# Optimization experiments

Hardware: AMD Instinct MI355X
Metric: run time of the kernel (lower is better)

The kernel has to match this reference:

```python
import jax, jax.numpy as jnp
import numpy as np


def _gru(x_seq, W_ih, W_hh, b_ih, b_hh):
    """Batched torch-style GRU. x_seq: [B,T,H] -> outputs [B,T,H].
    Gate order (torch.nn.GRU): r, z, n. n = tanh(xn + r*(W_hn h + b_hn))."""
    B, T, H = x_seq.shape
    # precompute input projections for all timesteps: [B,T,3H]
    xp = jnp.einsum('bth,gh->btg', x_seq, W_ih) + b_ih

    def step(h, xt):  # h: [B,H], xt: [B,3H]
        hp = h @ W_hh.T + b_hh  # [B,3H]
        xr, xz, xn = jnp.split(xt, 3, axis=-1)
        hr, hz, hn = jnp.split(hp, 3, axis=-1)
        r = jax.nn.sigmoid(xr + hr)
        z = jax.nn.sigmoid(xz + hz)
        n = jnp.tanh(xn + r * hn)
        h_new = (1.0 - z) * n + z * h
        return h_new, h_new

    h0 = jnp.zeros((B, H), dtype=x_seq.dtype)
    _, hs = jax.lax.scan(step, h0, jnp.swapaxes(xp, 0, 1))  # [T,B,H]
    return jnp.swapaxes(hs, 0, 1)


def setup_inputs() -> dict:
    key = jax.random.key(0)
    B, T, C, H, D = 128, 64, 8000, 256, 16
    G = 3 * H
    ks = jax.random.split(key, 32)
    s = 0.05  # scale for stable params
    inp = {
        'x': (jax.random.uniform(ks[0], (B, T, C)) < 0.01).astype(jnp.float32),  # sparse multi-hot
        'demographic': jax.random.normal(ks[1], (B, D), jnp.float32),
        'embed_W': jax.random.normal(ks[2], (H, C), jnp.float32) * s,
        'embed_b': jax.random.normal(ks[3], (H,), jnp.float32) * s,
        'aW_ih': jax.random.normal(ks[4], (G, H), jnp.float32) * s,
        'aW_hh': jax.random.normal(ks[5], (G, H), jnp.float32) * s,
        'ab_ih': jax.random.normal(ks[6], (G,), jnp.float32) * s,
        'ab_hh': jax.random.normal(ks[7], (G,), jnp.float32) * s,
        'bW_ih': jax.random.normal(ks[8], (G, H), jnp.float32) * s,
        'bW_hh': jax.random.normal(ks[9], (G, H), jnp.float32) * s,
        'bb_ih': jax.random.normal(ks[10], (G,), jnp.float32) * s,
        'bb_hh': jax.random.normal(ks[11], (G,), jnp.float32) * s,
        'attnA_W': jax.random.normal(ks[12], (1, H), jnp.float32) * s,
        'attnA_b': jax.random.normal(ks[13], (1,), jnp.float32) * s,
        'attnB_W': jax.random.normal(ks[14], (H, H), jnp.float32) * s,
        'attnB_b': jax.random.normal(ks[15], (H,), jnp.float32) * s,
        'cls_W1': jax.random.normal(ks[16], (H, H + D), jnp.float32) * s,
        'cls_b1': jax.random.normal(ks[17], (H,), jnp.float32) * s,
        'cls_W2': jax.random.normal(ks[18], (C, H), jnp.float32) * s,
        'cls_b2': jax.random.normal(ks[19], (C,), jnp.float32) * s,
        'dl_W1': jax.random.normal(ks[20], (H, H + D), jnp.float32) * s,
        'dl_b1': jax.random.normal(ks[21], (H,), jnp.float32) * s,
        'dl_W2': jax.random.normal(ks[22], (1, H), jnp.float32) * s,
        'dl_b2': jax.random.normal(ks[23], (1,), jnp.float32) * s,
    }
    return inp


def reference(x, demographic, embed_W, embed_b,
              aW_ih, aW_hh, ab_ih, ab_hh,
              bW_ih, bW_hh, bb_ih, bb_hh,
              attnA_W, attnA_b, attnB_W, attnB_b,
              cls_W1, cls_b1, cls_W2, cls_b2,
              dl_W1, dl_b1, dl_W2, dl_b2):
    # code embedding: [B,T,C] @ [C,H] -> [B,T,H]
    embedded = jnp.einsum('btc,hc->bth', x, embed_W) + embed_b

    alpha_out = _gru(embedded, aW_ih, aW_hh, ab_ih, ab_hh)  # [B,T,H]
    beta_out = _gru(embedded, bW_ih, bW_hh, bb_ih, bb_hh)   # [B,T,H]

    e_alpha = jnp.einsum('bth,oh->bto', alpha_out, attnA_W)[..., 0] + attnA_b[0]  # [B,T]
    alpha = jax.nn.softmax(e_alpha, axis=1)                                       # [B,T]
    beta = jnp.tanh(jnp.einsum('bth,gh->btg', beta_out, attnB_W) + attnB_b)       # [B,T,H]

    context = jnp.einsum('bth,bt->bh', embedded * beta, alpha)  # [B,H]

    combined = jnp.concatenate([context, demographic], axis=1)  # [B,H+D]
    # classifier (dropout = identity, eval mode)
    h1 = jax.nn.relu(combined @ cls_W1.T + cls_b1)
    logits = h1 @ cls_W2.T + cls_b2                              # [B,C]
    # death/LOS head
    h2 = jax.nn.relu(combined @ dl_W1.T + dl_b1)
    dl_logit = h2 @ dl_W2.T + dl_b2                              # [B,1]

    return jnp.concatenate([logits, dl_logit], axis=1)          # [B,C+1]
```

## Files before the change

### kernel.cpp

```cpp
#include <hip/hip_runtime.h>


typedef __attribute__((ext_vector_type(4))) float f32x4;
typedef __attribute__((ext_vector_type(8))) short short8;

__device__ inline short f2bf(float f) {
  unsigned u = __float_as_uint(f);
  u += 0x7fffu + ((u >> 16) & 1u);
  return (short)(u >> 16);
}
__device__ inline float bf2f(short u) {
  return __uint_as_float(((unsigned)(unsigned short)u) << 16);
}
__device__ inline float sigf(float x) { return 1.f / (1.f + __expf(-x)); }
__device__ inline float tanh_fast(float x) {
  x = fminf(fmaxf(x, -15.f), 15.f);
  float e = __expf(2.f * x);
  return (e - 1.f) / (e + 1.f);
}

__global__ void transpose_w(const float* __restrict__ in, float* __restrict__ outT) {
  __shared__ float tile[32][33];
  const int tx = threadIdx.x, ty = threadIdx.y;
  const int c0 = blockIdx.x * 32, h0 = blockIdx.y * 32;
#pragma unroll
  for (int k = 0; k < 4; ++k)
    tile[ty * 4 + k][tx] = in[(long)(h0 + ty * 4 + k) * 8000 + c0 + tx];
  __syncthreads();
#pragma unroll
  for (int k = 0; k < 4; ++k)
    outT[(long)(c0 + ty * 4 + k) * 256 + h0 + tx] = tile[tx][ty * 4 + k];
}

__global__ __launch_bounds__(512) void pad_pack(const float* __restrict__ w1,
                                                const float* __restrict__ w1d,
                                                float* __restrict__ o1,
                                                float* __restrict__ o2,
                                                const float* __restrict__ aWhh,
                                                const float* __restrict__ bWhh,
                                                short* __restrict__ wbf) {
  const int bid = blockIdx.x;
  if (bid < 288) {
    int idx = bid * 512 + threadIdx.x;
    int half = idx / (256 * 288);
    int r = idx % (256 * 288);
    int n = r / 288, k = r % 288;
    float v = (k < 272) ? (half ? w1d[n * 272 + k] : w1[n * 272 + k]) : 0.f;
    if (half) o2[r] = v; else o1[r] = v;
  } else {
    const int F = (bid - 288) * 512 + threadIdx.x;
    int f = F;
    const int lane = f & 63; f >>= 6;
    const int w = f & 15; f >>= 4;
    const int e = f % 3; f /= 3;
    const int kt = f & 7; f >>= 3;
    const int gru = f;
    const float* W = gru ? bWhh : aWhh;
    const int g = e * 256 + w * 16 + (lane & 15);
    const int k = kt * 32 + (lane >> 4) * 8;
    const float* p = W + (long)g * 256 + k;
    short8 v;
#pragma unroll
    for (int j = 0; j < 8; ++j) v[j] = f2bf(p[j]);
    *(short8*)(wbf + (long)F * 8) = v;
  }
}

__global__ __launch_bounds__(256) void embed_sparse(const float* __restrict__ x,
                                                    const float* __restrict__ Wt,
                                                    const float* __restrict__ eb,
                                                    float* __restrict__ emb) {
  __shared__ int sidx[512];
  __shared__ float sval[512];
  __shared__ int scnt;
  const int bt = blockIdx.x;
  const int tid = threadIdx.x;
  if (tid == 0) scnt = 0;
  __syncthreads();
  const float* xr = x + (long)bt * 8000;
  for (int i = tid; i < 2000; i += 256) {
    float4 v = ((const float4*)xr)[i];
    if (v.x != 0.f) { int p = atomicAdd(&scnt, 1); if (p < 512) { sidx[p] = i * 4 + 0; sval[p] = v.x; } }
    if (v.y != 0.f) { int p = atomicAdd(&scnt, 1); if (p < 512) { sidx[p] = i * 4 + 1; sval[p] = v.y; } }
    if (v.z != 0.f) { int p = atomicAdd(&scnt, 1); if (p < 512) { sidx[p] = i * 4 + 2; sval[p] = v.z; } }
    if (v.w != 0.f) { int p = atomicAdd(&scnt, 1); if (p < 512) { sidx[p] = i * 4 + 3; sval[p] = v.w; } }
  }
  __syncthreads();
  const int n = min(scnt, 512);
  float acc = eb[tid];
  for (int i = 0; i < n; ++i) acc += sval[i] * Wt[(long)sidx[i] * 256 + tid];
  emb[(long)bt * 256 + tid] = acc;
}

__global__ __launch_bounds__(256) void gemm_bt(const float* __restrict__ A,
                                               const float* __restrict__ B,
                                               const float* __restrict__ bias,
                                               float* __restrict__ C,
                                               int M, int N, int K, int ldc, int act) {
  __shared__ short As[64][40];
  __shared__ short Bs[64][40];
  const int tid = threadIdx.x;
  const int lane = tid & 63, wave = tid >> 6;
  const int wm = wave >> 1, wn = wave & 1;
  const int l15 = lane & 15, lhi = lane >> 4;
  const int m0 = blockIdx.y * 64, n0 = blockIdx.x * 64;
  const int srow = tid >> 2, scol = (tid & 3) * 8;
  f32x4 acc[2][2];
#pragma unroll
  for (int i = 0; i < 2; ++i)
#pragma unroll
    for (int j = 0; j < 2; ++j) acc[i][j] = (f32x4){0.f, 0.f, 0.f, 0.f};

  for (int k0 = 0; k0 < K; k0 += 32) {
    __syncthreads();
    {
      const float* p = A + (long)(m0 + srow) * K + k0 + scol;
      float4 f0 = *(const float4*)p;
      float4 f1 = *(const float4*)(p + 4);
      short8 v;
      v[0] = f2bf(f0.x); v[1] = f2bf(f0.y); v[2] = f2bf(f0.z); v[3] = f2bf(f0.w);
      v[4] = f2bf(f1.x); v[5] = f2bf(f1.y); v[6] = f2bf(f1.z); v[7] = f2bf(f1.w);
      *(short8*)&As[srow][scol] = v;
      const float* q = B + (long)(n0 + srow) * K + k0 + scol;
      float4 g0 = *(const float4*)q;
      float4 g1 = *(const float4*)(q + 4);
      short8 u;
      u[0] = f2bf(g0.x); u[1] = f2bf(g0.y); u[2] = f2bf(g0.z); u[3] = f2bf(g0.w);
      u[4] = f2bf(g1.x); u[5] = f2bf(g1.y); u[6] = f2bf(g1.z); u[7] = f2bf(g1.w);
      *(short8*)&Bs[srow][scol] = u;
    }
    __syncthreads();
    short8 af0 = *(const short8*)&As[wm * 32 + l15][lhi * 8];
    short8 af1 = *(const short8*)&As[wm * 32 + 16 + l15][lhi * 8];
    short8 bf0 = *(const short8*)&Bs[wn * 32 + l15][lhi * 8];
    short8 bf1 = *(const short8*)&Bs[wn * 32 + 16 + l15][lhi * 8];
    acc[0][0] = __builtin_amdgcn_mfma_f32_16x16x32_bf16(af0, bf0, acc[0][0], 0, 0, 0);
    acc[0][1] = __builtin_amdgcn_mfma_f32_16x16x32_bf16(af0, bf1, acc[0][1], 0, 0, 0);
    acc[1][0] = __builtin_amdgcn_mfma_f32_16x16x32_bf16(af1, bf0, acc[1][0], 0, 0, 0);
    acc[1][1] = __builtin_amdgcn_mfma_f32_16x16x32_bf16(af1, bf1, acc[1][1], 0, 0, 0);
  }
#pragma unroll
  for (int j = 0; j < 2; ++j) {
    const int col = n0 + wn * 32 + j * 16 + l15;
    const float bv = bias[col];
#pragma unroll
    for (int i = 0; i < 2; ++i) {
#pragma unroll
      for (int r = 0; r < 4; ++r) {
        const int row = m0 + wm * 32 + i * 16 + lhi * 4 + r;
        float v = acc[i][j][r] + bv;
        if (act == 1) v = fmaxf(v, 0.f);
        else if (act == 2) v = tanh_fast(v);
        C[(long)row * ldc + col] = v;
      }
    }
  }
}

__global__ __launch_bounds__(256) void gemm_dual(const float* __restrict__ A,
                                                 const float* __restrict__ B1,
                                                 const float* __restrict__ B2,
                                                 const float* __restrict__ bias1,
                                                 const float* __restrict__ bias2,
                                                 short* __restrict__ C1,
                                                 short* __restrict__ C2,
                                                 int K) {
  __shared__ short As[64][40];
  __shared__ short Bs1[64][40];
  __shared__ short Bs2[64][40];
  const int tid = threadIdx.x;
  const int lane = tid & 63, wave = tid >> 6;
  const int wm = wave >> 1, wn = wave & 1;
  const int l15 = lane & 15, lhi = lane >> 4;
  const int m0 = blockIdx.y * 64, n0 = blockIdx.x * 64;
  const int srow = tid >> 2, scol = (tid & 3) * 8;
  f32x4 acc1[2][2], acc2[2][2];
#pragma unroll
  for (int i = 0; i < 2; ++i)
#pragma unroll
    for (int j = 0; j < 2; ++j) {
      acc1[i][j] = (f32x4){0.f, 0.f, 0.f, 0.f};
      acc2[i][j] = (f32x4){0.f, 0.f, 0.f, 0.f};
    }

  for (int k0 = 0; k0 < K; k0 += 32) {
    __syncthreads();
    {
      const float* p = A + (long)(m0 + srow) * K + k0 + scol;
      float4 f0 = *(const float4*)p;
      float4 f1 = *(const float4*)(p + 4);
      short8 v;
      v[0] = f2bf(f0.x); v[1] = f2bf(f0.y); v[2] = f2bf(f0.z); v[3] = f2bf(f0.w);
      v[4] = f2bf(f1.x); v[5] = f2bf(f1.y); v[6] = f2bf(f1.z); v[7] = f2bf(f1.w);
      *(short8*)&As[srow][scol] = v;
      const float* q1 = B1 + (long)(n0 + srow) * K + k0 + scol;
      float4 g0 = *(const float4*)q1;
      float4 g1 = *(const float4*)(q1 + 4);
      short8 u;
      u[0] = f2bf(g0.x); u[1] = f2bf(g0.y); u[2] = f2bf(g0.z); u[3] = f2bf(g0.w);
      u[4] = f2bf(g1.x); u[5] = f2bf(g1.y); u[6] = f2bf(g1.z); u[7] = f2bf(g1.w);
      *(short8*)&Bs1[srow][scol] = u;
      const float* q2 = B2 + (long)(n0 + srow) * K + k0 + scol;
      float4 h0 = *(const float4*)q2;
      float4 h1 = *(const float4*)(q2 + 4);
      short8 t;
      t[0] = f2bf(h0.x); t[1] = f2bf(h0.y); t[2] = f2bf(h0.z); t[3] = f2bf(h0.w);
      t[4] = f2bf(h1.x); t[5] = f2bf(h1.y); t[6] = f2bf(h1.z); t[7] = f2bf(h1.w);
      *(short8*)&Bs2[srow][scol] = t;
    }
    __syncthreads();
    short8 af0 = *(const short8*)&As[wm * 32 + l15][lhi * 8];
    short8 af1 = *(const short8*)&As[wm * 32 + 16 + l15][lhi * 8];
    short8 b10 = *(const short8*)&Bs1[wn * 32 + l15][lhi * 8];
    short8 b11 = *(const short8*)&Bs1[wn * 32 + 16 + l15][lhi * 8];
    short8 b20 = *(const short8*)&Bs2[wn * 32 + l15][lhi * 8];
    short8 b21 = *(const short8*)&Bs2[wn * 32 + 16 + l15][lhi * 8];
    acc1[0][0] = __builtin_amdgcn_mfma_f32_16x16x32_bf16(af0, b10, acc1[0][0], 0, 0, 0);
    acc1[0][1] = __builtin_amdgcn_mfma_f32_16x16x32_bf16(af0, b11, acc1[0][1], 0, 0, 0);
    acc1[1][0] = __builtin_amdgcn_mfma_f32_16x16x32_bf16(af1, b10, acc1[1][0], 0, 0, 0);
    acc1[1][1] = __builtin_amdgcn_mfma_f32_16x16x32_bf16(af1, b11, acc1[1][1], 0, 0, 0);
    acc2[0][0] = __builtin_amdgcn_mfma_f32_16x16x32_bf16(af0, b20, acc2[0][0], 0, 0, 0);
    acc2[0][1] = __builtin_amdgcn_mfma_f32_16x16x32_bf16(af0, b21, acc2[0][1], 0, 0, 0);
    acc2[1][0] = __builtin_amdgcn_mfma_f32_16x16x32_bf16(af1, b20, acc2[1][0], 0, 0, 0);
    acc2[1][1] = __builtin_amdgcn_mfma_f32_16x16x32_bf16(af1, b21, acc2[1][1], 0, 0, 0);
  }
#pragma unroll
  for (int j = 0; j < 2; ++j) {
    const int col = n0 + wn * 32 + j * 16 + l15;
    const float bv1 = bias1[col];
    const float bv2 = bias2[col];
#pragma unroll
    for (int i = 0; i < 2; ++i) {
#pragma unroll
      for (int r = 0; r < 4; ++r) {
        const int row = m0 + wm * 32 + i * 16 + lhi * 4 + r;
        C1[(long)row * 768 + col] = f2bf(acc1[i][j][r] + bv1);
        C2[(long)row * 768 + col] = f2bf(acc2[i][j][r] + bv2);
      }
    }
  }
}

__global__ __launch_bounds__(1024, 4)
void gru_scan(const short* __restrict__ xpa,
              const short* __restrict__ xpb,
              const short* __restrict__ wbf,
              const float* __restrict__ abhh,
              const float* __restrict__ bbhh,
              float* __restrict__ aout,
              float* __restrict__ bout) {
  const int tid = threadIdx.x;
  const int lane = tid & 63, w = tid >> 6;
  const int l15 = lane & 15, lhi = lane >> 4;
  const int gru = blockIdx.x >> 5, chunk = blockIdx.x & 31;
  const int b0 = chunk * 4;
  const short* xp  = gru ? xpb : xpa;
  const float* bhh = gru ? bbhh : abhh;
  float* outp = gru ? bout : aout;

  __shared__ short hl[2][16][264];
  __shared__ short xplb[2][4][768];
  __shared__ short wlds[16][3][64][8];

  auto FR = [&](int kt, int e) -> const short8* {
    return (const short8*)(wbf + ((((long)gru * 8 + kt) * 3 + e) * 16 + w) * 512 + (long)lane * 8);
  };

  short8 wf[3][5];
#pragma unroll
  for (int e = 0; e < 3; ++e)
#pragma unroll
    for (int kt = 0; kt < 5; ++kt) wf[e][kt] = *FR(kt, e);
#pragma unroll
  for (int e = 0; e < 3; ++e) *(short8*)&wlds[w][e][lane][0] = *FR(5, e);

  float bh[3];
#pragma unroll
  for (int e = 0; e < 3; ++e) bh[e] = bhh[e * 256 + w * 16 + l15];

  for (int i = tid; i < 2 * 16 * 264; i += 1024) (&hl[0][0][0])[i] = 0;

  auto STAGE = [&](int par, int tt) {
    if (w < 6) {
      const int c = w * 64 + lane;
      const int b = c / 96, off8 = (c % 96) * 8;
      const short* gp = xp + ((long)(b0 + b) * 64 + tt) * 768 + off8;
      __builtin_amdgcn_global_load_lds((const __attribute__((address_space(1))) unsigned int*)gp,
                                       (__attribute__((address_space(3))) unsigned int*)((short*)&xplb[par][0][0] + (long)w * 512),
                                       16, 0, 0);
    }
  };
  STAGE(0, 0);
  __syncthreads();

  float hreg = 0.f;
  const int col = w * 16 + l15;

  for (int t = 0; t < 64; ++t) {
    const int cur = t & 1;
    short8 s60 = *FR(6, 0), s61 = *FR(6, 1), s62 = *FR(6, 2);
    short8 s70 = *FR(7, 0), s71 = *FR(7, 1), s72 = *FR(7, 2);
    if (t + 1 < 64) STAGE(cur ^ 1, t + 1);

    f32x4 acc[3];
#pragma unroll
    for (int e = 0; e < 3; ++e) acc[e] = (f32x4){0.f, 0.f, 0.f, 0.f};
#pragma unroll
    for (int kt = 0; kt < 5; ++kt) {
      short8 a = *(const short8*)&hl[cur][l15][kt * 32 + lhi * 8];
      acc[0] = __builtin_amdgcn_mfma_f32_16x16x32_bf16(a, wf[0][kt], acc[0], 0, 0, 0);
      acc[1] = __builtin_amdgcn_mfma_f32_16x16x32_bf16(a, wf[1][kt], acc[1], 0, 0, 0);
      acc[2] = __builtin_amdgcn_mfma_f32_16x16x32_bf16(a, wf[2][kt], acc[2], 0, 0, 0);
    }
    {
      short8 a = *(const short8*)&hl[cur][l15][5 * 32 + lhi * 8];
#pragma unroll
      for (int e = 0; e < 3; ++e) {
        short8 wl = *(const short8*)&wlds[w][e][lane][0];
        acc[e] = __builtin_amdgcn_mfma_f32_16x16x32_bf16(a, wl, acc[e], 0, 0, 0);
      }
    }
    {
      short8 a = *(const short8*)&hl[cur][l15][6 * 32 + lhi * 8];
      acc[0] = __builtin_amdgcn_mfma_f32_16x16x32_bf16(a, s60, acc[0], 0, 0, 0);
      acc[1] = __builtin_amdgcn_mfma_f32_16x16x32_bf16(a, s61, acc[1], 0, 0, 0);
      acc[2] = __builtin_amdgcn_mfma_f32_16x16x32_bf16(a, s62, acc[2], 0, 0, 0);
    }
    {
      short8 a = *(const short8*)&hl[cur][l15][7 * 32 + lhi * 8];
      acc[0] = __builtin_amdgcn_mfma_f32_16x16x32_bf16(a, s70, acc[0], 0, 0, 0);
      acc[1] = __builtin_amdgcn_mfma_f32_16x16x32_bf16(a, s71, acc[1], 0, 0, 0);
      acc[2] = __builtin_amdgcn_mfma_f32_16x16x32_bf16(a, s72, acc[2], 0, 0, 0);
    }

    {
      const float xr = bf2f(xplb[cur][lhi][col]);
      const float xz = bf2f(xplb[cur][lhi][256 + col]);
      const float xn = bf2f(xplb[cur][lhi][512 + col]);
      const float r = sigf(xr + acc[0][0] + bh[0]);
      const float z = sigf(xz + acc[1][0] + bh[1]);
      const float n = tanh_fast(xn + r * (acc[2][0] + bh[2]));
      const float hn = (1.f - z) * n + z * hreg;
      hreg = hn;
      hl[cur ^ 1][lhi << 2][col] = f2bf(hn);
      outp[((long)(b0 + lhi) * 64 + t) * 256 + col] = hn;
    }
    __syncthreads();
  }
}

__global__ __launch_bounds__(256) void alpha_ctx(const float* __restrict__ aout,
                                                 const float* __restrict__ aW,
                                                 const float* __restrict__ ab,
                                                 const float* __restrict__ emb,
                                                 const float* __restrict__ beta,
                                                 const float* __restrict__ demo,
                                                 float* __restrict__ comb) {
  __shared__ float part[64][4];
  __shared__ float al[64];
  const int b = blockIdx.x, tid = threadIdx.x;
  const int t = tid >> 2, q = tid & 3;
  const float* p = aout + (long)(b * 64 + t) * 256 + q * 64;
  const float* wv = aW + q * 64;
  float s = 0.f;
  for (int i = 0; i < 64; ++i) s += p[i] * wv[i];
  part[t][q] = s;
  __syncthreads();
  if (tid < 64) {
    float e = part[tid][0] + part[tid][1] + part[tid][2] + part[tid][3] + ab[0];
    float m = e;
    for (int k = 32; k; k >>= 1) m = fmaxf(m, __shfl_xor(m, k));
    float ex = __expf(e - m);
    float sum = ex;
    for (int k = 32; k; k >>= 1) sum += __shfl_xor(sum, k);
    al[tid] = ex / sum;
  }
  __syncthreads();
  const int h = tid;
  float acc = 0.f;
  for (int t2 = 0; t2 < 64; ++t2) {
    const long ix = (long)(b * 64 + t2) * 256 + h;
    acc += al[t2] * emb[ix] * beta[ix];
  }
  comb[b * 288 + h] = acc;
  if (h < 16) comb[b * 288 + 256 + h] = demo[b * 16 + h];
  else if (h < 32) comb[b * 288 + 256 + h] = 0.f;
}

__global__ __launch_bounds__(64) void dl_head(const float* __restrict__ h2,
                                              const float* __restrict__ w,
                                              const float* __restrict__ bias,
                                              float* __restrict__ out) {
  const int b = blockIdx.x, lane = threadIdx.x;
  float s = 0.f;
#pragma unroll
  for (int i = 0; i < 4; ++i) s += h2[b * 256 + lane * 4 + i] * w[lane * 4 + i];
  for (int k = 32; k; k >>= 1) s += __shfl_xor(s, k);
  if (lane == 0) out[(long)b * 8001 + 8000] = s + bias[0];
}

extern "C" void kernel_launch(void* const* d_in, const int* in_sizes, int n_in,
                              void* d_out, int out_size, void* d_ws, size_t ws_size,
                              hipStream_t stream) {
  (void)in_sizes; (void)n_in; (void)out_size; (void)ws_size;
  const float* x      = (const float*)d_in[0];
  const float* demo   = (const float*)d_in[1];
  const float* embW   = (const float*)d_in[2];
  const float* embB   = (const float*)d_in[3];
  const float* aWih   = (const float*)d_in[4];
  const float* aWhh   = (const float*)d_in[5];
  const float* abih   = (const float*)d_in[6];
  const float* abhh   = (const float*)d_in[7];
  const float* bWih   = (const float*)d_in[8];
  const float* bWhh   = (const float*)d_in[9];
  const float* bbih   = (const float*)d_in[10];
  const float* bbhh   = (const float*)d_in[11];
  const float* attnAW = (const float*)d_in[12];
  const float* attnAb = (const float*)d_in[13];
  const float* attnBW = (const float*)d_in[14];
  const float* attnBb = (const float*)d_in[15];
  const float* clsW1  = (const float*)d_in[16];
  const float* clsb1  = (const float*)d_in[17];
  const float* clsW2  = (const float*)d_in[18];
  const float* clsb2  = (const float*)d_in[19];
  const float* dlW1   = (const float*)d_in[20];
  const float* dlb1   = (const float*)d_in[21];
  const float* dlW2   = (const float*)d_in[22];
  const float* dlb2   = (const float*)d_in[23];
  float* out = (float*)d_out;
  float* ws = (float*)d_ws;

  float* Wt    = ws;
  float* emb   = Wt + 2048000;
  short* xpa16 = (short*)(emb + 2097152);
  short* xpb16 = xpa16 + 6291456;
  float* aoutB = (float*)(xpb16 + 6291456);
  float* boutB = aoutB + 2097152;
  float* betaB = boutB + 2097152;
  float* comb  = betaB + 2097152;
  float* h1    = comb + 36864;
  float* h2    = h1 + 32768;
  float* W1p   = h2 + 32768;
  float* W1pd  = W1p + 73728;
  short* wbf   = (short*)(W1pd + 73728);

  transpose_w<<<dim3(250, 8), dim3(32, 8), 0, stream>>>(embW, Wt);
  pad_pack<<<dim3(384), dim3(512), 0, stream>>>(clsW1, dlW1, W1p, W1pd, aWhh, bWhh, wbf);
  embed_sparse<<<dim3(8192), dim3(256), 0, stream>>>(x, Wt, embB, emb);
  gemm_dual<<<dim3(12, 128), dim3(256), 0, stream>>>(emb, aWih, bWih, abih, bbih, xpa16, xpb16, 256);
  gru_scan<<<dim3(64), dim3(1024), 0, stream>>>(xpa16, xpb16, wbf, abhh, bbhh, aoutB, boutB);
  gemm_bt<<<dim3(4, 128), dim3(256), 0, stream>>>(boutB, attnBW, attnBb, betaB, 8192, 256, 256, 256, 2);
  alpha_ctx<<<dim3(128), dim3(256), 0, stream>>>(aoutB, attnAW, attnAb, emb, betaB, demo, comb);
  gemm_bt<<<dim3(4, 2), dim3(256), 0, stream>>>(comb, W1p, clsb1, h1, 128, 256, 288, 256, 1);
  gemm_bt<<<dim3(4, 2), dim3(256), 0, stream>>>(comb, W1pd, dlb1, h2, 128, 256, 288, 256, 1);
  gemm_bt<<<dim3(125, 2), dim3(256), 0, stream>>>(h1, clsW2, clsb2, out, 128, 8000, 256, 8001, 0);
  dl_head<<<dim3(128), dim3(64), 0, stream>>>(h2, dlW2, dlb2, out);
}
```

Before: 267.0 us.

## Store intermediates in bf16 and pre-convert GEMM weights once

Measured after the change: 255.4 us. -4.4%, faster.

```diff
diff --git a/kernel.cpp b/kernel.cpp
--- a/kernel.cpp
+++ b/kernel.cpp
@@ -38,7 +38,13 @@
                                                 float* __restrict__ o2,
                                                 const float* __restrict__ aWhh,
                                                 const float* __restrict__ bWhh,
-                                                short* __restrict__ wbf) {
+                                                short* __restrict__ wbf,
+                                                const float* __restrict__ aWih,
+                                                const float* __restrict__ bWih,
+                                                const float* __restrict__ attnBW,
+                                                short* __restrict__ wih16a,
+                                                short* __restrict__ wih16b,
+                                                short* __restrict__ attnBW16) {
   const int bid = blockIdx.x;
   if (bid < 288) {
     int idx = bid * 512 + threadIdx.x;
@@ -47,7 +53,7 @@
     int n = r / 288, k = r % 288;
     float v = (k < 272) ? (half ? w1d[n * 272 + k] : w1[n * 272 + k]) : 0.f;
     if (half) o2[r] = v; else o1[r] = v;
-  } else {
+  } else if (bid < 384) {
     const int F = (bid - 288) * 512 + threadIdx.x;
     int f = F;
     const int lane = f & 63; f >>= 6;
@@ -63,13 +69,18 @@
 #pragma unroll
     for (int j = 0; j < 8; ++j) v[j] = f2bf(p[j]);
     *(short8*)(wbf + (long)F * 8) = v;
+  } else {
+    const int i = (bid - 384) * 512 + threadIdx.x;
+    if (i < 196608) wih16a[i] = f2bf(aWih[i]);
+    else if (i < 393216) wih16b[i - 196608] = f2bf(bWih[i - 196608]);
+    else attnBW16[i - 393216] = f2bf(attnBW[i - 393216]);
   }
 }
 
 __global__ __launch_bounds__(256) void embed_sparse(const float* __restrict__ x,
                                                     const float* __restrict__ Wt,
                                                     const float* __restrict__ eb,
-                                                    float* __restrict__ emb) {
+                                                    short* __restrict__ emb16) {
   __shared__ int sidx[512];
   __shared__ float sval[512];
   __shared__ int scnt;
@@ -89,7 +100,7 @@
   const int n = min(scnt, 512);
   float acc = eb[tid];
   for (int i = 0; i < n; ++i) acc += sval[i] * Wt[(long)sidx[i] * 256 + tid];
-  emb[(long)bt * 256 + tid] = acc;
+  emb16[(long)bt * 256 + tid] = f2bf(acc);
 }
 
 __global__ __launch_bounds__(256) void gemm_bt(const float* __restrict__ A,
@@ -157,14 +168,14 @@
   }
 }
 
-__global__ __launch_bounds__(256) void gemm_dual(const float* __restrict__ A,
-                                                 const float* __restrict__ B1,
-                                                 const float* __restrict__ B2,
-                                                 const float* __restrict__ bias1,
-                                                 const float* __restrict__ bias2,
-                                                 short* __restrict__ C1,
-                                                 short* __restrict__ C2,
-                                                 int K) {
+__global__ __launch_bounds__(256) void gemm_dual16(const short* __restrict__ A,
+                                                   const short* __restrict__ B1,
+                                                   const short* __restrict__ B2,
+                                                   const float* __restrict__ bias1,
+                                                   const float* __restrict__ bias2,
+                                                   short* __restrict__ C1,
+                                                   short* __restrict__ C2,
+                                                   int K) {
   __shared__ short As[64][40];
   __shared__ short Bs1[64][40];
   __shared__ short Bs2[64][40];
@@ -186,27 +197,9 @@
   for (int k0 = 0; k0 < K; k0 += 32) {
     __syncthreads();
     {
-      const float* p = A + (long)(m0 + srow) * K + k0 + scol;
-      float4 f0 = *(const float4*)p;
-      float4 f1 = *(const float4*)(p + 4);
-      short8 v;
-      v[0] = f2bf(f0.x); v[1] = f2bf(f0.y); v[2] = f2bf(f0.z); v[3] = f2bf(f0.w);
-      v[4] = f2bf(f1.x); v[5] = f2bf(f1.y); v[6] = f2bf(f1.z); v[7] = f2bf(f1.w);
-      *(short8*)&As[srow][scol] = v;
-      const float* q1 = B1 + (long)(n0 + srow) * K + k0 + scol;
-      float4 g0 = *(const float4*)q1;
-      float4 g1 = *(const float4*)(q1 + 4);
-      short8 u;
-      u[0] = f2bf(g0.x); u[1] = f2bf(g0.y); u[2] = f2bf(g0.z); u[3] = f2bf(g0.w);
-      u[4] = f2bf(g1.x); u[5] = f2bf(g1.y); u[6] = f2bf(g1.z); u[7] = f2bf(g1.w);
-      *(short8*)&Bs1[srow][scol] = u;
-      const float* q2 = B2 + (long)(n0 + srow) * K + k0 + scol;
-      float4 h0 = *(const float4*)q2;
-      float4 h1 = *(const float4*)(q2 + 4);
-      short8 t;
-      t[0] = f2bf(h0.x); t[1] = f2bf(h0.y); t[2] = f2bf(h0.z); t[3] = f2bf(h0.w);
-      t[4] = f2bf(h1.x); t[5] = f2bf(h1.y); t[6] = f2bf(h1.z); t[7] = f2bf(h1.w);
-      *(short8*)&Bs2[srow][scol] = t;
+      *(short8*)&As[srow][scol]  = *(const short8*)(A  + (long)(m0 + srow) * K + k0 + scol);
+      *(short8*)&Bs1[srow][scol] = *(const short8*)(B1 + (long)(n0 + srow) * K + k0 + scol);
+      *(short8*)&Bs2[srow][scol] = *(const short8*)(B2 + (long)(n0 + srow) * K + k0 + scol);
     }
     __syncthreads();
     short8 af0 = *(const short8*)&As[wm * 32 + l15][lhi * 8];
@@ -241,14 +234,68 @@
   }
 }
 
+__global__ __launch_bounds__(256) void gemm16_bt(const short* __restrict__ A,
+                                                 const short* __restrict__ B,
+                                                 const float* __restrict__ bias,
+                                                 float* __restrict__ C,
+                                                 int N_, int K, int ldc, int act) {
+  __shared__ short As[64][40];
+  __shared__ short Bs[64][40];
+  const int tid = threadIdx.x;
+  const int lane = tid & 63, wave = tid >> 6;
+  const int wm = wave >> 1, wn = wave & 1;
+  const int l15 = lane & 15, lhi = lane >> 4;
+  const int m0 = blockIdx.y * 64, n0 = blockIdx.x * 64;
+  const int srow = tid >> 2, scol = (tid & 3) * 8;
+  f32x4 acc[2][2];
+#pragma unroll
+  for (int i = 0; i < 2; ++i)
+#pragma unroll
+    for (int j = 0; j < 2; ++j) acc[i][j] = (f32x4){0.f, 0.f, 0.f, 0.f};
+
+  for (int k0 = 0; k0 < K; k0 += 32) {
+    __syncthreads();
+    {
+      *(short8*)&As[srow][scol] = *(const short8*)(A + (long)(m0 + srow) * K + k0 + scol);
+      *(short8*)&Bs[srow][scol] = *(const short8*)(B + (long)(n0 + srow) * K + k0 + scol);
+    }
+    __syncthreads();
+    short8 af0 = *(const short8*)&As[wm * 32 + l15][lhi * 8];
+    short8 af1 = *(const short8*)&As[wm * 32 + 16 + l15][lhi * 8];
+    short8 bf0 = *(const short8*)&Bs[wn * 32 + l15][lhi * 8];
+    short8 bf1 = *(const short8*)&Bs[wn * 32 + 16 + l15][lhi * 8];
+    acc[0][0] = __builtin_amdgcn_mfma_f32_16x16x32_bf16(af0, bf0, acc[0][0], 0, 0, 0);
+    acc[0][1] = __builtin_amdgcn_mfma_f32_16x16x32_bf16(af0, bf1, acc[0][1], 0, 0, 0);
+    acc[1][0] = __builtin_amdgcn_mfma_f32_16x16x32_bf16(af1, bf0, acc[1][0], 0, 0, 0);
+    acc[1][1] = __builtin_amdgcn_mfma_f32_16x16x32_bf16(af1, bf1, acc[1][1], 0, 0, 0);
+  }
+#pragma unroll
+  for (int j = 0; j < 2; ++j) {
+    const int col = n0 + wn * 32 + j * 16 + l15;
+    const float bv = bias[col];
+#pragma unroll
+    for (int i = 0; i < 2; ++i) {
+#pragma unroll
+      for (int r = 0; r < 4; ++r) {
+        const int row = m0 + wm * 32 + i * 16 + lhi * 4 + r;
+        float v = acc[i][j][r] + bv;
+        if (act == 1) v = fmaxf(v, 0.f);
+        else if (act == 2) v = tanh_fast(v);
+        C[(long)row * ldc + col] = v;
+      }
+    }
+  }
+  (void)N_;
+}
+
 __global__ __launch_bounds__(1024, 4)
 void gru_scan(const short* __restrict__ xpa,
               const short* __restrict__ xpb,
               const short* __restrict__ wbf,
               const float* __restrict__ abhh,
               const float* __restrict__ bbhh,
-              float* __restrict__ aout,
-              float* __restrict__ bout) {
+              short* __restrict__ aout,
+              short* __restrict__ bout) {
   const int tid = threadIdx.x;
   const int lane = tid & 63, w = tid >> 6;
   const int l15 = lane & 15, lhi = lane >> 4;
@@ -256,7 +303,7 @@
   const int b0 = chunk * 4;
   const short* xp  = gru ? xpb : xpa;
   const float* bhh = gru ? bbhh : abhh;
-  float* outp = gru ? bout : aout;
+  short* outp = gru ? bout : aout;
 
   __shared__ short hl[2][16][264];
   __shared__ short xplb[2][4][768];
@@ -342,17 +389,18 @@
       const float n = tanh_fast(xn + r * (acc[2][0] + bh[2]));
       const float hn = (1.f - z) * n + z * hreg;
       hreg = hn;
-      hl[cur ^ 1][lhi << 2][col] = f2bf(hn);
-      outp[((long)(b0 + lhi) * 64 + t) * 256 + col] = hn;
-    }
-    __syncthreads();
-  }
-}
-
-__global__ __launch_bounds__(256) void alpha_ctx(const float* __restrict__ aout,
+      const short hb = f2bf(hn);
+      hl[cur ^ 1][lhi << 2][col] = hb;
+      outp[((long)(b0 + lhi) * 64 + t) * 256 + col] = hb;
+    }
+    __syncthreads();
+  }
+}
+
+__global__ __launch_bounds__(256) void alpha_ctx(const short* __restrict__ aout16,
                                                  const float* __restrict__ aW,
                                                  const float* __restrict__ ab,
-                                                 const float* __restrict__ emb,
+                                                 const short* __restrict__ emb16,
                                                  const float* __restrict__ beta,
                                                  const float* __restrict__ demo,
                                                  float* __restrict__ comb) {
@@ -360,10 +408,10 @@
   __shared__ float al[64];
   const int b = blockIdx.x, tid = threadIdx.x;
   const int t = tid >> 2, q = tid & 3;
-  const float* p = aout + (long)(b * 64 + t) * 256 + q * 64;
+  const short* p = aout16 + (long)(b * 64 + t) * 256 + q * 64;
   const float* wv = aW + q * 64;
   float s = 0.f;
-  for (int i = 0; i < 64; ++i) s += p[i] * wv[i];
+  for (int i = 0; i < 64; ++i) s += bf2f(p[i]) * wv[i];
   part[t][q] = s;
   __syncthreads();
   if (tid < 64) {
@@ -380,7 +428,7 @@
   float acc = 0.f;
   for (int t2 = 0; t2 < 64; ++t2) {
     const long ix = (long)(b * 64 + t2) * 256 + h;
-    acc += al[t2] * emb[ix] * beta[ix];
+    acc += al[t2] * bf2f(emb16[ix]) * beta[ix];
   }
   comb[b * 288 + h] = acc;
   if (h < 16) comb[b * 288 + 256 + h] = demo[b * 16 + h];
@@ -430,27 +478,32 @@
   float* out = (float*)d_out;
   float* ws = (float*)d_ws;
 
-  float* Wt    = ws;
-  float* emb   = Wt + 2048000;
-  short* xpa16 = (short*)(emb + 2097152);
-  short* xpb16 = xpa16 + 6291456;
-  float* aoutB = (float*)(xpb16 + 6291456);
-  float* boutB = aoutB + 2097152;
-  float* betaB = boutB + 2097152;
-  float* comb  = betaB + 2097152;
-  float* h1    = comb + 36864;
-  float* h2    = h1 + 32768;
-  float* W1p   = h2 + 32768;
-  float* W1pd  = W1p + 73728;
-  short* wbf   = (short*)(W1pd + 73728);
+  float* Wt      = ws;
+  short* emb16   = (short*)(Wt + 2048000);
+  short* xpa16   = emb16 + 2097152;
+  short* xpb16   = xpa16 + 6291456;
+  short* aout16  = xpb16 + 6291456;
+  short* bout16  = aout16 + 2097152;
+  float* betaB   = (float*)(bout16 + 2097152);
+  float* comb    = betaB + 2097152;
+  float* h1      = comb + 36864;
+  float* h2      = h1 + 32768;
+  float* W1p     = h2 + 32768;
+  float* W1pd    = W1p + 73728;
+  short* wbf     = (short*)(W1pd + 73728);
+  short* wih16a  = wbf + 393216;
+  short* wih16b  = wih16a + 196608;
+  short* attnBW16 = wih16b + 196608;
 
   transpose_w<<<dim3(250, 8), dim3(32, 8), 0, stream>>>(embW, Wt);
-  pad_pack<<<dim3(384), dim3(512), 0, stream>>>(clsW1, dlW1, W1p, W1pd, aWhh, bWhh, wbf);
-  embed_sparse<<<dim3(8192), dim3(256), 0, stream>>>(x, Wt, embB, emb);
-  gemm_dual<<<dim3(12, 128), dim3(256), 0, stream>>>(emb, aWih, bWih, abih, bbih, xpa16, xpb16, 256);
-  gru_scan<<<dim3(64), dim3(1024), 0, stream>>>(xpa16, xpb16, wbf, abhh, bbhh, aoutB, boutB);
-  gemm_bt<<<dim3(4, 128), dim3(256), 0, stream>>>(boutB, attnBW, attnBb, betaB, 8192, 256, 256, 256, 2);
-  alpha_ctx<<<dim3(128), dim3(256), 0, stream>>>(aoutB, attnAW, attnAb, emb, betaB, demo, comb);
+  pad_pack<<<dim3(1280), dim3(512), 0, stream>>>(clsW1, dlW1, W1p, W1pd, aWhh, bWhh, wbf,
+                                                 aWih, bWih, attnBW, wih16a, wih16b, attnBW16);
+  embed_sparse<<<dim3(8192), dim3(256), 0, stream>>>(x, Wt, embB, emb16);
+  gemm_dual16<<<dim3(12, 128), dim3(256), 0, stream>>>(emb16, wih16a, wih16b, abih, bbih,
+                                                       xpa16, xpb16, 256);
+  gru_scan<<<dim3(64), dim3(1024), 0, stream>>>(xpa16, xpb16, wbf, abhh, bbhh, aout16, bout16);
+  gemm16_bt<<<dim3(4, 128), dim3(256), 0, stream>>>(bout16, attnBW16, attnBb, betaB, 256, 256, 256, 2);
+  alpha_ctx<<<dim3(128), dim3(256), 0, stream>>>(aout16, attnAW, attnAb, emb16, betaB, demo, comb);
   gemm_bt<<<dim3(4, 2), dim3(256), 0, stream>>>(comb, W1p, clsb1, h1, 128, 256, 288, 256, 1);
   gemm_bt<<<dim3(4, 2), dim3(256), 0, stream>>>(comb, W1pd, dlb1, h2, 128, 256, 288, 256, 1);
   gemm_bt<<<dim3(125, 2), dim3(256), 0, stream>>>(h1, clsW2, clsb2, out, 128, 8000, 256, 8001, 0);
```
